# Optimization experiments

Measured on AMD Instinct MI355X. Metric: run time of the kernel, lower is better.

The kernel has to match this reference:

```python
import jax, jax.numpy as jnp
import numpy as np

DIM, HEADS, SEQ_LEN = 768, 12, 4096
HEAD_DIM = DIM // HEADS
RMS_EPS = 1.1920928955078125e-07  # torch fp32 finfo eps (default for F.rms_norm)
ATTN_SCALE = 0.12


def _rms_norm(x):
    # F.rms_norm(x, (x.size(-1),)) with no weight
    return x * jax.lax.rsqrt(jnp.mean(x * x, axis=-1, keepdims=True) + RMS_EPS)


def _rotary_tables(T, head_dim):
    # angular_freq: (1/1024)**linspace(0,1,head_dim//4) padded with zeros to head_dim//2
    freqs = (1.0 / 1024.0) ** jnp.linspace(0.0, 1.0, head_dim // 4, dtype=jnp.float32)
    freqs = jnp.concatenate([freqs, jnp.zeros(head_dim // 4, dtype=jnp.float32)])
    t = jnp.arange(T, dtype=jnp.float32)
    theta = t[:, None] * freqs[None, :]  # [T, head_dim//2]
    return jnp.cos(theta), jnp.sin(theta)


def _apply_rotary(x, cos, sin):
    # x: [B, T, H, D]; cos/sin: [T, D//2]
    x1, x2 = jnp.split(x.astype(jnp.float32), 2, axis=-1)
    c = cos[None, :, None, :]
    s = sin[None, :, None, :]
    y1 = x1 * c + x2 * s
    y2 = -x1 * s + x2 * c
    return jnp.concatenate([y1, y2], axis=-1).astype(x.dtype)


def setup_inputs() -> dict:
    key = jax.random.key(0)
    k1, k2, k3 = jax.random.split(key, 3)
    x = jax.random.normal(k1, (1, SEQ_LEN, DIM), dtype=jnp.float32)
    std = 0.5 * DIM ** (-0.5)
    bound = (3.0 ** 0.5) * std
    qkv_w = jax.random.uniform(k2, (3, DIM, DIM), dtype=jnp.float32, minval=-bound, maxval=bound)
    # c_proj is zero-initialized in the module; use small random weights for a nontrivial baseline
    c_proj_w = jax.random.normal(k3, (DIM, DIM), dtype=jnp.float32) * (DIM ** -0.5)
    return {"x": x, "qkv_w": qkv_w, "c_proj_w": c_proj_w}


def reference(x, qkv_w, c_proj_w):
    B, T, dim = x.shape
    H, D = HEADS, HEAD_DIM
    # fused QKV: F.linear(x, qkv_w.flatten(end_dim=1)) -> x @ W^T, split into q,k,v
    qkv = jnp.einsum('btd,kfd->btkf', x, qkv_w)  # [B, T, 3, dim]
    qkv = qkv.reshape(B, T, 3, H, D)
    q, k, v = qkv[:, :, 0], qkv[:, :, 1], qkv[:, :, 2]  # each [B, T, H, D]
    q, k = _rms_norm(q), _rms_norm(k)
    cos, sin = _rotary_tables(T, D)
    q, k = _apply_rotary(q, cos, sin), _apply_rotary(k, cos, sin)
    # causal attention with scale=0.12 (flex_attention with causal block mask)
    scores = jnp.einsum('bthd,bshd->bhts', q, k) * ATTN_SCALE  # [B, H, T, T]
    causal = jnp.tril(jnp.ones((T, T), dtype=bool))
    scores = jnp.where(causal[None, None], scores, jnp.finfo(scores.dtype).min)
    probs = jax.nn.softmax(scores, axis=-1)
    y = jnp.einsum('bhts,bshd->bthd', probs, v).reshape(B, T, dim)
    return y @ c_proj_w.T
```

## Files before the change

kernel.cpp:

```cpp
#include <hip/hip_runtime.h>
#include <math.h>


typedef __bf16 bf16;
typedef __bf16 bf16x4 __attribute__((ext_vector_type(4)));
typedef __bf16 bf16x8 __attribute__((ext_vector_type(8)));
typedef float  f32x4  __attribute__((ext_vector_type(4)));

#define MFMA_BF16(a, b, c) __builtin_amdgcn_mfma_f32_16x16x32_bf16((a), (b), (c), 0, 0, 0)

#define SEQ  4096
#define NH   12
#define HD   64
#define DM   768
#define NQKV 2304
#define NPART 4
#define ATTN_SCALE 0.12f
#define LOG2E 1.4426950408889634f
#define RMS_EPS 1.1920928955078125e-07f

typedef __attribute__((address_space(3))) void  lds_void;
typedef const __attribute__((address_space(1))) void g_void;

__device__ __forceinline__ void gload16(const void* g, void* l)
{
  __builtin_amdgcn_global_load_lds((g_void*)g, (lds_void*)l, 16, 0, 0);
}

__global__ __launch_bounds__(256) void convert_all(
    const float* __restrict__ s0, bf16* __restrict__ d0, int n0,
    const float* __restrict__ s1, bf16* __restrict__ d1, int n1,
    const float* __restrict__ s2, bf16* __restrict__ d2, int n2)
{
  int b = blockIdx.x;
  const int b0 = n0 >> 11, b1 = n1 >> 11;
  const float* s; bf16* d;
  if (b < b0)            { s = s0; d = d0; }
  else if (b < b0 + b1)  { s = s1; d = d1; b -= b0; }
  else                   { s = s2; d = d2; b -= b0 + b1; }
  const int i0 = (b * 256 + threadIdx.x) * 8;
  f32x4 a = *(const f32x4*)(s + i0);
  f32x4 c = *(const f32x4*)(s + i0 + 4);
  bf16x8 o;
#pragma unroll
  for (int j = 0; j < 4; j++) { o[j] = (bf16)a[j]; o[j + 4] = (bf16)c[j]; }
  *(bf16x8*)(d + i0) = o;
}

__device__ __forceinline__ void gemm128_core(
    const bf16* __restrict__ A, const bf16* __restrict__ B,
    int m0, int n0, bf16 (*As)[128][32], bf16 (*Bs)[128][32], f32x4 acc[4][4])
{
  const int tid = threadIdx.x;
  const int lane = tid & 63, w = tid >> 6;
  const int c16 = lane & 15, q4 = lane >> 4;
  const int mo = (w & 1) * 64, no = (w >> 1) * 64;
  const int srow = tid >> 2, scol = (tid & 3) * 8;
  const f32x4 vzero = {0.f, 0.f, 0.f, 0.f};
#pragma unroll
  for (int i = 0; i < 4; i++)
#pragma unroll
    for (int j = 0; j < 4; j++) acc[i][j] = vzero;

  const bf16* aBase = A + (size_t)(m0 + srow) * DM + scol;
  const bf16* bBase = B + (size_t)(n0 + srow) * DM + scol;

#define STAGE128(buf, kk) do {                                          \
    gload16(aBase + (kk),                   &As[buf][srow][scol]);      \
    gload16(aBase + (size_t)64 * DM + (kk), &As[buf][srow + 64][scol]); \
    gload16(bBase + (kk),                   &Bs[buf][srow][scol]);      \
    gload16(bBase + (size_t)64 * DM + (kk), &Bs[buf][srow + 64][scol]); \
  } while (0)

  STAGE128(0, 0);
  __syncthreads();
  int cur = 0;
  for (int k0 = 0; k0 < DM; k0 += 32) {
    const int kn = k0 + 32;
    if (kn < DM) STAGE128(cur ^ 1, kn);
    bf16x8 ar[4], br[4];
#pragma unroll
    for (int mq = 0; mq < 4; mq++)
      ar[mq] = *(const bf16x8*)&As[cur][mo + mq * 16 + c16][q4 * 8];
#pragma unroll
    for (int nq = 0; nq < 4; nq++)
      br[nq] = *(const bf16x8*)&Bs[cur][no + nq * 16 + c16][q4 * 8];
    __builtin_amdgcn_s_setprio(1);
#pragma unroll
    for (int mq = 0; mq < 4; mq++)
#pragma unroll
      for (int nq = 0; nq < 4; nq++)
        acc[mq][nq] = MFMA_BF16(ar[mq], br[nq], acc[mq][nq]);
    __builtin_amdgcn_s_setprio(0);
    __syncthreads();
    cur ^= 1;
  }
#undef STAGE128
}

__global__ __launch_bounds__(256) void gemm_qkv(
    const bf16* __restrict__ A, const bf16* __restrict__ B,
    bf16* __restrict__ Qb, bf16* __restrict__ Kb, bf16* __restrict__ Vt)
{
  __shared__ bf16 As[2][128][32];
  __shared__ bf16 Bs[2][128][32];
  const int m0 = blockIdx.x * 128, n0 = blockIdx.y * 128;
  f32x4 acc[4][4];
  gemm128_core(A, B, m0, n0, As, Bs, acc);

  const int lane = threadIdx.x & 63, w = threadIdx.x >> 6;
  const int c16 = lane & 15, q4 = lane >> 4;
  const int mo = (w & 1) * 64, no = (w >> 1) * 64;
  const int kidx = blockIdx.y / 6;
  const int rr0 = (n0 - kidx * DM) + no;
  const int h = rr0 >> 6;

  if (kidx == 2) {
#pragma unroll
    for (int nq = 0; nq < 4; nq++) {
      const int d = nq * 16 + c16;
#pragma unroll
      for (int mq = 0; mq < 4; mq++) {
        const int mb = m0 + mo + mq * 16 + q4 * 4;
#pragma unroll
        for (int rg = 0; rg < 4; rg++)
          Vt[((h * HD) + d) * SEQ + mb + rg] = (bf16)acc[mq][nq][rg];
      }
    }
  } else {
    bf16* dst = kidx ? Kb : Qb;
    const float scale = kidx ? 1.0f : (ATTN_SCALE * LOG2E);
    const float fr = exp2f(-10.0f * (float)c16 * (1.0f / 15.0f));
#pragma unroll
    for (int mq = 0; mq < 4; mq++) {
#pragma unroll
      for (int rg = 0; rg < 4; rg++) {
        const int m = m0 + mo + mq * 16 + q4 * 4 + rg;
        const float x0 = acc[mq][0][rg], x1 = acc[mq][1][rg];
        const float x2 = acc[mq][2][rg], x3 = acc[mq][3][rg];
        float ss = x0 * x0 + x1 * x1 + x2 * x2 + x3 * x3;
        ss += __shfl_xor(ss, 1, 64);
        ss += __shfl_xor(ss, 2, 64);
        ss += __shfl_xor(ss, 4, 64);
        ss += __shfl_xor(ss, 8, 64);
        const float rinv = rsqrtf(ss * (1.0f / 64.0f) + RMS_EPS) * scale;
        const float xn0 = x0 * rinv, xn1 = x1 * rinv;
        const float xn2 = x2 * rinv, xn3 = x3 * rinv;
        float sn, cs;
        sincosf((float)m * fr, &sn, &cs);
        const float y0 = xn0 * cs + xn2 * sn;
        const float y2 = xn2 * cs - xn0 * sn;
        bf16* rp = dst + (size_t)(h * SEQ + m) * HD + c16;
        rp[0]  = (bf16)y0;
        rp[16] = (bf16)xn1;
        rp[32] = (bf16)y2;
        rp[48] = (bf16)xn3;
      }
    }
  }
}

__global__ __launch_bounds__(256) void gemm_proj(
    const bf16* __restrict__ Opart, const float* __restrict__ Lpart,
    const bf16* __restrict__ B, float* __restrict__ C)
{
  __shared__ bf16 As[2][64][32];
  __shared__ bf16 Bs[2][64][32];
  __shared__ float invs[NH * 64];
  const int m0 = blockIdx.x * 64, n0 = blockIdx.y * 64;
  const int tid = threadIdx.x;
  const int lane = tid & 63, w = tid >> 6;
  const int c16 = lane & 15, q4 = lane >> 4;
  const int mo = (w & 1) * 32, no = (w >> 1) * 32;
  const int srow = tid >> 2, scol = (tid & 3) * 8;
  const int qi = m0 >> 7;
  const int rbase = m0 & 64;
  const int r128 = rbase + srow;
  const f32x4 vzero = {0.f, 0.f, 0.f, 0.f};
  f32x4 acc[2][2];
#pragma unroll
  for (int i = 0; i < 2; i++)
#pragma unroll
    for (int j = 0; j < 2; j++) acc[i][j] = vzero;

  const bf16* bBase = B + (size_t)(n0 + srow) * DM + scol;

#define ALOAD(kk, r0, r1, r2, r3) do {                                        \
    const int h_ = (kk) >> 6;                                                 \
    const bf16* ab_ = Opart + (size_t)((h_ * 32 + qi) * NPART) * 8192         \
                      + r128 * 64 + ((kk) & 63) + scol;                       \
    r0 = *(const bf16x8*)(ab_);                                               \
    r1 = *(const bf16x8*)(ab_ + 8192);                                        \
    r2 = *(const bf16x8*)(ab_ + 16384);                                       \
    r3 = *(const bf16x8*)(ab_ + 24576);                                       \
  } while (0)

#define AWRITE(buf, kk, r0, r1, r2, r3) do {                                  \
    const float iv_ = invs[(((kk) >> 6) << 6) + srow];                        \
    bf16x8 y_;                                                                \
    _Pragma("unroll")                                                         \
    for (int e = 0; e < 8; e++)                                               \
      y_[e] = (bf16)(((float)r0[e] + (float)r1[e] + (float)r2[e]              \
                      + (float)r3[e]) * iv_);                                 \
    *(bf16x8*)&As[buf][srow][scol] = y_;                                      \
  } while (0)

  bf16x8 p0, p1, p2, p3;
  ALOAD(0, p0, p1, p2, p3);
  gload16(bBase, &Bs[0][srow][scol]);
  for (int idx = tid; idx < NH * 64; idx += 256) {
    const int h = idx >> 6, r = idx & 63;
    const int u0 = (h * 32 + qi) * NPART;
    float ls = 0.f;
#pragma unroll
    for (int p = 0; p < NPART; p++) ls += Lpart[(u0 + p) * 128 + rbase + r];
    invs[idx] = 1.0f / ls;
  }
  __syncthreads();
  AWRITE(0, 0, p0, p1, p2, p3);
  __syncthreads();

  int cur = 0;
  for (int k0 = 0; k0 < DM; k0 += 32) {
    const int kn = k0 + 32;
    if (kn < DM) {
      ALOAD(kn, p0, p1, p2, p3);
      gload16(bBase + kn, &Bs[cur ^ 1][srow][scol]);
    }
    bf16x8 ar[2], br[2];
#pragma unroll
    for (int mq = 0; mq < 2; mq++)
      ar[mq] = *(const bf16x8*)&As[cur][mo + mq * 16 + c16][q4 * 8];
#pragma unroll
    for (int nq = 0; nq < 2; nq++)
      br[nq] = *(const bf16x8*)&Bs[cur][no + nq * 16 + c16][q4 * 8];
    __builtin_amdgcn_s_setprio(1);
#pragma unroll
    for (int mq = 0; mq < 2; mq++)
#pragma unroll
      for (int nq = 0; nq < 2; nq++)
        acc[mq][nq] = MFMA_BF16(ar[mq], br[nq], acc[mq][nq]);
    __builtin_amdgcn_s_setprio(0);
    if (kn < DM) AWRITE(cur ^ 1, kn, p0, p1, p2, p3);
    __syncthreads();
    cur ^= 1;
  }
#undef ALOAD
#undef AWRITE

#pragma unroll
  for (int nq = 0; nq < 2; nq++) {
    const int n = n0 + no + nq * 16 + c16;
#pragma unroll
    for (int mq = 0; mq < 2; mq++) {
      const int mb = m0 + mo + mq * 16 + q4 * 4;
#pragma unroll
      for (int rg = 0; rg < 4; rg++)
        C[(size_t)(mb + rg) * DM + n] = acc[mq][nq][rg];
    }
  }
}

__global__ __launch_bounds__(256, 3) void flash_partial(
    const bf16* __restrict__ Qb, const bf16* __restrict__ Kb,
    const bf16* __restrict__ Vt, bf16* __restrict__ Opart,
    float* __restrict__ Lpart)
{
  __shared__ bf16 Ks[64][72];
  __shared__ bf16 Vts[64][72];
  __shared__ bf16 Pst[4][32][68];
  const int id = blockIdx.x;
  const int swz = (id & 7) * 96 + (id >> 3);
  const int h = swz >> 6;
  const int rrem = swz & 63;
  const int p = rrem >> 4;
  const int jb = rrem & 15;
  const int tid = threadIdx.x;
  const int lane = tid & 63, w = tid >> 6;
  const int c16 = lane & 15, q4 = lane >> 4;
  const int sr = tid >> 3, sc8 = (tid & 7) * 8;

  const bf16* Kbase = Kb + (size_t)h * SEQ * HD;
  const bf16* Vbase = Vt + (size_t)h * HD * SEQ;
  const f32x4 vzero = {0.f, 0.f, 0.f, 0.f};

#pragma unroll 1
  for (int half = 0; half < 2; ++half) {
    const int qi = half ? jb : (31 - jb);
    const int q0 = qi * 128;

    bf16x8 aq[2][2];
#pragma unroll
    for (int f = 0; f < 2; f++) {
      const int tq = q0 + w * 32 + f * 16 + c16;
      aq[f][0] = *(const bf16x8*)&Qb[((h * SEQ) + tq) * HD + q4 * 8];
      aq[f][1] = *(const bf16x8*)&Qb[((h * SEQ) + tq) * HD + 32 + q4 * 8];
    }
    const int qg[2] = { q0 + w * 32 + c16, q0 + w * 32 + 16 + c16 };
    const int qb[2] = { q0 + w * 32,       q0 + w * 32 + 16 };

    f32x4 O[2][4];
    float l_f[2] = {0.f, 0.f};
#pragma unroll
    for (int f = 0; f < 2; f++)
#pragma unroll
      for (int j = 0; j < 4; j++) O[f][j] = vzero;

    const int sEnd = q0 + 64;
    const int sBeg = p * 64;
    if (sBeg <= sEnd) {
      bf16x8 kr0 = *(const bf16x8*)&Kbase[(sBeg + sr) * HD + sc8];
      bf16x8 kr1 = *(const bf16x8*)&Kbase[(sBeg + sr + 32) * HD + sc8];
      bf16x8 vr0 = *(const bf16x8*)&Vbase[sr * SEQ + sBeg + sc8];
      bf16x8 vr1 = *(const bf16x8*)&Vbase[(sr + 32) * SEQ + sBeg + sc8];

      for (int s0 = sBeg; s0 <= sEnd; s0 += NPART * 64) {
        __syncthreads();
        *(bf16x8*)&Ks[sr][sc8]       = kr0;
        *(bf16x8*)&Ks[sr + 32][sc8]  = kr1;
        *(bf16x8*)&Vts[sr][sc8]      = vr0;
        *(bf16x8*)&Vts[sr + 32][sc8] = vr1;
        __syncthreads();

        const int snext = s0 + NPART * 64;
        if (snext <= sEnd) {
          kr0 = *(const bf16x8*)&Kbase[(snext + sr) * HD + sc8];
          kr1 = *(const bf16x8*)&Kbase[(snext + sr + 32) * HD + sc8];
          vr0 = *(const bf16x8*)&Vbase[sr * SEQ + snext + sc8];
          vr1 = *(const bf16x8*)&Vbase[(sr + 32) * SEQ + snext + sc8];
        }

        bf16x8 kf0[4], kf1[4];
#pragma unroll
        for (int nt = 0; nt < 4; nt++) {
          kf0[nt] = *(const bf16x8*)&Ks[nt * 16 + c16][q4 * 8];
          kf1[nt] = *(const bf16x8*)&Ks[nt * 16 + c16][32 + q4 * 8];
        }
#pragma unroll
        for (int f = 0; f < 2; f++) {
          f32x4 S[4];
          __builtin_amdgcn_s_setprio(1);
#pragma unroll
          for (int nt = 0; nt < 4; nt++) {
            f32x4 z = vzero;
            z = MFMA_BF16(kf0[nt], aq[f][0], z);
            z = MFMA_BF16(kf1[nt], aq[f][1], z);
            S[nt] = z;
          }
          __builtin_amdgcn_s_setprio(0);
          float lf = l_f[f];
          if (s0 + 63 <= qb[f]) {
#pragma unroll
            for (int nt = 0; nt < 4; nt++) {
#pragma unroll
              for (int rg = 0; rg < 4; rg++) {
                const float pv = exp2f(S[nt][rg]);
                S[nt][rg] = pv;
                lf += pv;
              }
              bf16x4 pk = { (bf16)S[nt][0], (bf16)S[nt][1], (bf16)S[nt][2], (bf16)S[nt][3] };
              *(bf16x4*)&Pst[w][f * 16 + c16][nt * 16 + q4 * 4] = pk;
            }
          } else if (s0 > qb[f] + 15) {
            const bf16x4 zk = { (bf16)0.f, (bf16)0.f, (bf16)0.f, (bf16)0.f };
#pragma unroll
            for (int nt = 0; nt < 4; nt++)
              *(bf16x4*)&Pst[w][f * 16 + c16][nt * 16 + q4 * 4] = zk;
          } else {
#pragma unroll
            for (int nt = 0; nt < 4; nt++) {
#pragma unroll
              for (int rg = 0; rg < 4; rg++) {
                const int s_g = s0 + nt * 16 + q4 * 4 + rg;
                const float pv = (s_g > qg[f]) ? 0.f : exp2f(S[nt][rg]);
                S[nt][rg] = pv;
                lf += pv;
              }
              bf16x4 pk = { (bf16)S[nt][0], (bf16)S[nt][1], (bf16)S[nt][2], (bf16)S[nt][3] };
              *(bf16x4*)&Pst[w][f * 16 + c16][nt * 16 + q4 * 4] = pk;
            }
          }
          l_f[f] = lf;
        }
        bf16x8 ap[2][2];
#pragma unroll
        for (int f = 0; f < 2; f++) {
          ap[f][0] = *(const bf16x8*)&Pst[w][f * 16 + c16][q4 * 8];
          ap[f][1] = *(const bf16x8*)&Pst[w][f * 16 + c16][32 + q4 * 8];
        }
#pragma unroll
        for (int dt = 0; dt < 4; dt++) {
          bf16x8 bv0 = *(const bf16x8*)&Vts[dt * 16 + c16][q4 * 8];
          bf16x8 bv1 = *(const bf16x8*)&Vts[dt * 16 + c16][32 + q4 * 8];
          __builtin_amdgcn_s_setprio(1);
#pragma unroll
          for (int f = 0; f < 2; f++) {
            O[f][dt] = MFMA_BF16(ap[f][0], bv0, O[f][dt]);
            O[f][dt] = MFMA_BF16(ap[f][1], bv1, O[f][dt]);
          }
          __builtin_amdgcn_s_setprio(0);
        }
      }
    }

#pragma unroll
    for (int f = 0; f < 2; f++) {
      float l = l_f[f];
      l += __shfl_xor(l, 16, 64);
      l += __shfl_xor(l, 32, 64);
      l_f[f] = l;
    }
    const int u = ((h * 32 + qi) * NPART + p);
    bf16* Op = Opart + (size_t)u * 8192;
#pragma unroll
    for (int f = 0; f < 2; f++)
#pragma unroll
      for (int dt = 0; dt < 4; dt++)
#pragma unroll
        for (int rg = 0; rg < 4; rg++)
          Op[(w * 32 + f * 16 + q4 * 4 + rg) * 64 + dt * 16 + c16] = (bf16)O[f][dt][rg];
    if (lane < 32) {
      if (q4 == 0) {
#pragma unroll
        for (int f = 0; f < 2; f++)
          Lpart[u * 128 + w * 32 + f * 16 + c16] = l_f[f];
      }
    }
  }
}

extern "C" void kernel_launch(void* const* d_in, const int* in_sizes, int n_in,
                              void* d_out, int out_size, void* d_ws, size_t ws_size,
                              hipStream_t stream)
{
  (void)in_sizes; (void)n_in; (void)out_size; (void)ws_size;
  const float* x      = (const float*)d_in[0];
  const float* qkvw   = (const float*)d_in[1];
  const float* cprojw = (const float*)d_in[2];
  float* outp = (float*)d_out;

  const int NX = SEQ * DM, NW = NQKV * DM, NP = DM * DM;

  char* ws = (char*)d_ws;
  bf16*  xb    = (bf16*)(ws);
  bf16*  wqkv  = (bf16*)(ws + 6291456);
  bf16*  wproj = (bf16*)(ws + 9830400);
  bf16*  Q     = (bf16*)(ws + 11010048);
  bf16*  K     = (bf16*)(ws + 17301504);
  bf16*  Vt    = (bf16*)(ws + 23592960);
  bf16*  Opart = (bf16*)(ws + 29884416);
  float* Lpart = (float*)(ws + 55050240);

  convert_all<<<dim3((NX + NW + NP) / 2048), 256, 0, stream>>>(
      x, xb, NX, qkvw, wqkv, NW, cprojw, wproj, NP);

  gemm_qkv     <<<dim3(SEQ / 128, NQKV / 128), 256, 0, stream>>>(xb, wqkv, Q, K, Vt);
  flash_partial<<<dim3(16 * NH * NPART),       256, 0, stream>>>(Q, K, Vt, Opart, Lpart);
  gemm_proj    <<<dim3(SEQ / 64, DM / 64),     256, 0, stream>>>(Opart, Lpart, wproj, outp);
}
```

Baseline: 168.4 us.

## Prefetch two stages in out-proj GEMM and compute softmax row sums via MFMA

The output-projection GEMM now holds two register sets of A-tile loads and is unrolled by two, so global loads for tile k+2 are issued while tile k is computed. This deepens the prefetch to hide load latency, at the cost of more registers. In the flash kernel, the per-row softmax denominator is no longer summed with scalar adds and cross-lane shuffles. Instead it is accumulated by extra MFMAs of P against a ones-column vector. This moves the summation onto the matrix units but sums the bf16-rounded probabilities, which slightly changes numerics, and adds MFMA work per tile.

```diff
diff --git a/kernel.cpp b/kernel.cpp
--- a/kernel.cpp
+++ b/kernel.cpp
@@ -205,8 +205,29 @@
     *(bf16x8*)&As[buf][srow][scol] = y_;                                      \
   } while (0)
 
-  bf16x8 p0, p1, p2, p3;
-  ALOAD(0, p0, p1, p2, p3);
+#define MFMA_STEP(cb) do {                                                    \
+    bf16x8 ar[2], br[2];                                                      \
+    _Pragma("unroll")                                                         \
+    for (int mq = 0; mq < 2; mq++)                                            \
+      ar[mq] = *(const bf16x8*)&As[cb][mo + mq * 16 + c16][q4 * 8];           \
+    _Pragma("unroll")                                                         \
+    for (int nq = 0; nq < 2; nq++)                                            \
+      br[nq] = *(const bf16x8*)&Bs[cb][no + nq * 16 + c16][q4 * 8];           \
+    __builtin_amdgcn_s_setprio(1);                                            \
+    _Pragma("unroll")                                                         \
+    for (int mq = 0; mq < 2; mq++)                                            \
+      _Pragma("unroll")                                                       \
+      for (int nq = 0; nq < 2; nq++)                                          \
+        acc[mq][nq] = MFMA_BF16(ar[mq], br[nq], acc[mq][nq]);                 \
+    __builtin_amdgcn_s_setprio(0);                                            \
+  } while (0)
+
+  const int NT = DM / 32;
+
+  bf16x8 ra0, ra1, ra2, ra3;
+  bf16x8 rb0, rb1, rb2, rb3;
+  ALOAD(0,  ra0, ra1, ra2, ra3);
+  ALOAD(32, rb0, rb1, rb2, rb3);
   gload16(bBase, &Bs[0][srow][scol]);
   for (int idx = tid; idx < NH * 64; idx += 256) {
     const int h = idx >> 6, r = idx & 63;
@@ -217,36 +238,31 @@
     invs[idx] = 1.0f / ls;
   }
   __syncthreads();
-  AWRITE(0, 0, p0, p1, p2, p3);
+  AWRITE(0, 0, ra0, ra1, ra2, ra3);
   __syncthreads();
 
   int cur = 0;
-  for (int k0 = 0; k0 < DM; k0 += 32) {
-    const int kn = k0 + 32;
-    if (kn < DM) {
-      ALOAD(kn, p0, p1, p2, p3);
-      gload16(bBase + kn, &Bs[cur ^ 1][srow][scol]);
-    }
-    bf16x8 ar[2], br[2];
-#pragma unroll
-    for (int mq = 0; mq < 2; mq++)
-      ar[mq] = *(const bf16x8*)&As[cur][mo + mq * 16 + c16][q4 * 8];
-#pragma unroll
-    for (int nq = 0; nq < 2; nq++)
-      br[nq] = *(const bf16x8*)&Bs[cur][no + nq * 16 + c16][q4 * 8];
-    __builtin_amdgcn_s_setprio(1);
-#pragma unroll
-    for (int mq = 0; mq < 2; mq++)
-#pragma unroll
-      for (int nq = 0; nq < 2; nq++)
-        acc[mq][nq] = MFMA_BF16(ar[mq], br[nq], acc[mq][nq]);
-    __builtin_amdgcn_s_setprio(0);
-    if (kn < DM) AWRITE(cur ^ 1, kn, p0, p1, p2, p3);
+  for (int u = 0; u < NT; u += 2) {
+    if (u + 2 < NT) ALOAD((u + 2) * 32, ra0, ra1, ra2, ra3);
+    if (u + 1 < NT) {
+      AWRITE(cur ^ 1, (u + 1) * 32, rb0, rb1, rb2, rb3);
+      gload16(bBase + (u + 1) * 32, &Bs[cur ^ 1][srow][scol]);
+    }
+    MFMA_STEP(cur);
     __syncthreads();
     cur ^= 1;
+    if (u + 3 < NT) ALOAD((u + 3) * 32, rb0, rb1, rb2, rb3);
+    if (u + 2 < NT) {
+      AWRITE(cur ^ 1, (u + 2) * 32, ra0, ra1, ra2, ra3);
+      gload16(bBase + (u + 2) * 32, &Bs[cur ^ 1][srow][scol]);
+    }
+    MFMA_STEP(cur);
+    __syncthreads();
+    cur ^= 1;
   }
 #undef ALOAD
 #undef AWRITE
+#undef MFMA_STEP
 
 #pragma unroll
   for (int nq = 0; nq < 2; nq++) {
@@ -284,6 +300,11 @@
   const bf16* Vbase = Vt + (size_t)h * HD * SEQ;
   const f32x4 vzero = {0.f, 0.f, 0.f, 0.f};
 
+  const bf16 bv1 = (c16 == 0) ? (bf16)1.0f : (bf16)0.0f;
+  bf16x8 bone;
+#pragma unroll
+  for (int e = 0; e < 8; e++) bone[e] = bv1;
+
 #pragma unroll 1
   for (int half = 0; half < 2; ++half) {
     const int qi = half ? jb : (31 - jb);
@@ -300,7 +321,7 @@
     const int qb[2] = { q0 + w * 32,       q0 + w * 32 + 16 };
 
     f32x4 O[2][4];
-    float l_f[2] = {0.f, 0.f};
+    f32x4 acc_l[2] = {vzero, vzero};
 #pragma unroll
     for (int f = 0; f < 2; f++)
 #pragma unroll
@@ -348,16 +369,11 @@
             S[nt] = z;
           }
           __builtin_amdgcn_s_setprio(0);
-          float lf = l_f[f];
           if (s0 + 63 <= qb[f]) {
 #pragma unroll
             for (int nt = 0; nt < 4; nt++) {
 #pragma unroll
-              for (int rg = 0; rg < 4; rg++) {
-                const float pv = exp2f(S[nt][rg]);
-                S[nt][rg] = pv;
-                lf += pv;
-              }
+              for (int rg = 0; rg < 4; rg++) S[nt][rg] = exp2f(S[nt][rg]);
               bf16x4 pk = { (bf16)S[nt][0], (bf16)S[nt][1], (bf16)S[nt][2], (bf16)S[nt][3] };
               *(bf16x4*)&Pst[w][f * 16 + c16][nt * 16 + q4 * 4] = pk;
             }
@@ -372,15 +388,12 @@
 #pragma unroll
               for (int rg = 0; rg < 4; rg++) {
                 const int s_g = s0 + nt * 16 + q4 * 4 + rg;
-                const float pv = (s_g > qg[f]) ? 0.f : exp2f(S[nt][rg]);
-                S[nt][rg] = pv;
-                lf += pv;
+                S[nt][rg] = (s_g > qg[f]) ? 0.f : exp2f(S[nt][rg]);
               }
               bf16x4 pk = { (bf16)S[nt][0], (bf16)S[nt][1], (bf16)S[nt][2], (bf16)S[nt][3] };
               *(bf16x4*)&Pst[w][f * 16 + c16][nt * 16 + q4 * 4] = pk;
             }
           }
-          l_f[f] = lf;
         }
         bf16x8 ap[2][2];
 #pragma unroll
@@ -389,27 +402,25 @@
           ap[f][1] = *(const bf16x8*)&Pst[w][f * 16 + c16][32 + q4 * 8];
         }
 #pragma unroll
+        for (int f = 0; f < 2; f++) {
+          acc_l[f] = MFMA_BF16(ap[f][0], bone, acc_l[f]);
+          acc_l[f] = MFMA_BF16(ap[f][1], bone, acc_l[f]);
+        }
+#pragma unroll
         for (int dt = 0; dt < 4; dt++) {
           bf16x8 bv0 = *(const bf16x8*)&Vts[dt * 16 + c16][q4 * 8];
-          bf16x8 bv1 = *(const bf16x8*)&Vts[dt * 16 + c16][32 + q4 * 8];
+          bf16x8 bw1 = *(const bf16x8*)&Vts[dt * 16 + c16][32 + q4 * 8];
           __builtin_amdgcn_s_setprio(1);
 #pragma unroll
           for (int f = 0; f < 2; f++) {
             O[f][dt] = MFMA_BF16(ap[f][0], bv0, O[f][dt]);
-            O[f][dt] = MFMA_BF16(ap[f][1], bv1, O[f][dt]);
+            O[f][dt] = MFMA_BF16(ap[f][1], bw1, O[f][dt]);
           }
           __builtin_amdgcn_s_setprio(0);
         }
       }
     }
 
-#pragma unroll
-    for (int f = 0; f < 2; f++) {
-      float l = l_f[f];
-      l += __shfl_xor(l, 16, 64);
-      l += __shfl_xor(l, 32, 64);
-      l_f[f] = l;
-    }
     const int u = ((h * 32 + qi) * NPART + p);
     bf16* Op = Opart + (size_t)u * 8192;
 #pragma unroll
@@ -419,12 +430,12 @@
 #pragma unroll
         for (int rg = 0; rg < 4; rg++)
           Op[(w * 32 + f * 16 + q4 * 4 + rg) * 64 + dt * 16 + c16] = (bf16)O[f][dt][rg];
-    if (lane < 32) {
-      if (q4 == 0) {
-#pragma unroll
-        for (int f = 0; f < 2; f++)
-          Lpart[u * 128 + w * 32 + f * 16 + c16] = l_f[f];
-      }
+    if (c16 == 0) {
+#pragma unroll
+      for (int f = 0; f < 2; f++)
+#pragma unroll
+        for (int rg = 0; rg < 4; rg++)
+          Lpart[u * 128 + w * 32 + f * 16 + q4 * 4 + rg] = acc_l[f][rg];
     }
   }
 }
```

Result: slower. 172.0 us (+2.1%).
